# Performance work log

Measured on AMD Instinct MI355X. Metric: run time of the kernel, lower is better.

Reference implementation:

```python
import jax, jax.numpy as jnp
import numpy as np

EPS = 1e-6  # ieps_ln_default
B, S, H, DI, DO = 4, 4096, 8, 128, 128


def _ln(x, g, b, n_axes):
    """LayerNorm over the last n_axes dims (matches nn.LayerNorm(normalized_shape))."""
    axes = tuple(range(x.ndim - n_axes, x.ndim))
    mu = x.mean(axes, keepdims=True)
    var = x.var(axes, keepdims=True)
    return (x - mu) * jax.lax.rsqrt(var + EPS) * g + b


def setup_inputs() -> dict:
    key = jax.random.key(0)
    ks = jax.random.split(key, 12)
    sd = 0.02
    return {
        "heads_input": jax.random.normal(ks[0], (B, S, H, DI), jnp.float32),
        # GroupLinear trans_hid: per-head (2*DI -> 3*DO)
        "W_hid": jax.random.normal(ks[1], (H, 2 * DI, 3 * DO), jnp.float32) * sd,
        "b_hid": jnp.zeros((H, 3 * DO), jnp.float32),
        # normer_csum LN over (H, DI)
        "g_csum": jnp.ones((H, DI), jnp.float32),
        "beta_csum": jnp.zeros((H, DI), jnp.float32),
        # normer_hid LN over (H, 3, DO)
        "g_hid": jnp.ones((H, 3, DO), jnp.float32),
        "beta_hid": jnp.zeros((H, 3, DO), jnp.float32),
        # GroupLinear trans_og: per-head (DI + DO -> DO)
        "W_og": jax.random.normal(ks[2], (H, DI + DO, DO), jnp.float32) * sd,
        "b_og": jnp.zeros((H, DO), jnp.float32),
        # LN inside trans_og over (H, DO)
        "g_og": jnp.ones((H, DO), jnp.float32),
        "beta_og": jnp.zeros((H, DO), jnp.float32),
        "init_cx": jnp.zeros((H, DO), jnp.float32),
    }


def reference(heads_input, W_hid, b_hid, g_csum, beta_csum, g_hid, beta_hid,
              W_og, b_og, g_og, beta_og, init_cx):
    b, s, n, d = heads_input.shape
    # exclusive cumulative sum over seq: cat(zeros, x[:, :-1]).cumsum(1)
    csum = jnp.cumsum(heads_input, axis=1) - heads_input
    csum = _ln(csum, g_csum, beta_csum, 2)
    # grouped (per-head) linear producing igate/fgate/hidden
    x = jnp.concatenate([heads_input, csum], axis=-1)              # [b,s,n,2*d]
    h3 = jnp.einsum('bsni,nio->bsno', x, W_hid) + b_hid            # [b,s,n,3*do]
    do = h3.shape[-1] // 3
    h3 = _ln(h3.reshape(b, s, n, 3, do), g_hid, beta_hid, 3)
    igate, fgate, hidden = h3[..., 0, :], h3[..., 1, :], h3[..., 2, :]
    fg = jax.nn.sigmoid(fgate)
    igh = jax.nn.sigmoid(igate) * jax.nn.relu(hidden)
    # linear recurrence cell_t = fg_t * cell_{t-1} + igh_t  (LGateFunc, dim=1)
    c0 = jnp.broadcast_to(init_cx, (b, n, do))

    def step(c, fi):
        f, i = fi
        c = f * c + i
        return c, c

    _, cell = jax.lax.scan(step, c0, (jnp.swapaxes(fg, 0, 1), jnp.swapaxes(igh, 0, 1)))
    cell = jnp.swapaxes(cell, 0, 1)                                # [b,s,n,do]
    # output gate: GroupLinear + LN, then sigmoid * cell
    og_in = jnp.concatenate([heads_input, cell], axis=-1)
    og = jnp.einsum('bsni,nio->bsno', og_in, W_og) + b_og
    og = _ln(og, g_og, beta_og, 2)
    return jax.nn.sigmoid(og) * cell
```

## Files before the change

### kernel.cpp

```cpp
#include <hip/hip_runtime.h>
#include <math.h>

#define BB 4
#define SS 4096
#define HH 8
#define DI 128
#define DOo 128
#define HD 1024
#define NTOK (BB*SS)
#define LNEPS 1e-6f

#define CS1 32
#define NC1 128
#define CS2 128
#define NC2 32

typedef unsigned short ubf;
typedef __attribute__((ext_vector_type(8))) short    bf16x8;
typedef __attribute__((ext_vector_type(8))) unsigned short u16x8;
typedef __attribute__((ext_vector_type(4))) unsigned short u16x4;
typedef __attribute__((ext_vector_type(4))) float    f32x4;

__device__ __forceinline__ float bf2f(ubf x) {
    union { unsigned int u; float f; } v; v.u = ((unsigned int)x) << 16; return v.f;
}
__device__ __forceinline__ ubf f2bf(float f) {
    union { float f; unsigned int u; } v; v.f = f;
    unsigned int r = v.u + 0x7FFFu + ((v.u >> 16) & 1u);
    return (ubf)(r >> 16);
}
__device__ __forceinline__ float fast_sigmoid(float x) {
    return __builtin_amdgcn_rcpf(1.f + __expf(-x));
}
__device__ __forceinline__ void gload16(const ubf* g, ubf* l) {
    __builtin_amdgcn_global_load_lds(
        (const __attribute__((address_space(1))) void*)g,
        (__attribute__((address_space(3))) void*)l, 16, 0, 0);
}

__global__ void kwt_pack(const float* __restrict__ W, ubf* __restrict__ Wtp, int NB) {
    int bid = blockIdx.x;
    int ks = bid & 7;
    int ns = (bid >> 3) % (NB >> 6);
    int h  = bid / (8 * (NB >> 6));
    int t = threadIdx.x;
    int j = t >> 6, lane = t & 63;
    int n  = ns * 64 + j * 16 + (lane & 15);
    int k0 = ks * 32 + (lane >> 4) * 8;
    u16x8 o;
    #pragma unroll
    for (int e = 0; e < 8; ++e)
        o[e] = f2bf(W[((size_t)h * 256 + k0 + e) * NB + n]);
    *(u16x8*)(Wtp + ((((size_t)(h * (NB >> 6) + ns) * 8 + ks) * 4 + j) * 64 + lane) * 8) = o;
}

__global__ void k1_chunksum(const float* __restrict__ in, float* __restrict__ chunk,
                            ubf* __restrict__ in_bf) {
    int bid = blockIdx.x;
    int c = bid % NC1;
    int h = (bid / NC1) % HH;
    int b = bid / (NC1 * HH);
    int d = threadIdx.x;
    size_t base = (size_t)(b * SS + c * CS1) * HD + h * DI + d;
    float s = 0.f;
    for (int i = 0; i < CS1; ++i) {
        float v = in[base + (size_t)i * HD];
        in_bf[base + (size_t)i * HD] = f2bf(v);
        s += v;
    }
    chunk[((b * NC1 + c) * HH + h) * DI + d] = s;
}

__global__ void k2_chunkscan(float* __restrict__ chunk) {
    int bid = blockIdx.x;
    int h = bid % HH;
    int b = bid / HH;
    int d = threadIdx.x;
    float run = 0.f;
    for (int c0 = 0; c0 < NC1; c0 += 16) {
        float v[16];
        #pragma unroll
        for (int k = 0; k < 16; ++k)
            v[k] = chunk[((b * NC1 + c0 + k) * HH + h) * DI + d];
        #pragma unroll
        for (int k = 0; k < 16; ++k) {
            int idx = ((b * NC1 + c0 + k) * HH + h) * DI + d;
            chunk[idx] = run;
            run += v[k];
        }
    }
}

__global__ void __launch_bounds__(256) k3_csum_ln(
        const float* __restrict__ in, const float* __restrict__ chunkpre,
        const float* __restrict__ g, const float* __restrict__ beta,
        ubf* __restrict__ out) {
    __shared__ float2 scr[2][4];
    int c = blockIdx.x % NC1;
    int b = blockIdx.x / NC1;
    int t = threadIdx.x;
    int lane = t & 63, w = t >> 6;
    int d0 = t * 4;
    f32x4 run = *(const f32x4*)(chunkpre + (size_t)(b * NC1 + c) * HD + d0);
    f32x4 gg  = *(const f32x4*)(g + d0);
    f32x4 bb  = *(const f32x4*)(beta + d0);
    const float* pin = in + (size_t)(b * SS + c * CS1) * HD + d0;
    ubf* pout = out + (size_t)(b * SS + c * CS1) * HD + d0;

    f32x4 v = *(const f32x4*)(pin);
    for (int i = 0; i < CS1; ++i) {
        f32x4 cs = run;
        run += v;
        float s = cs[0] + cs[1] + cs[2] + cs[3];
        float q = cs[0]*cs[0] + cs[1]*cs[1] + cs[2]*cs[2] + cs[3]*cs[3];
        #pragma unroll
        for (int off = 32; off >= 1; off >>= 1) {
            s += __shfl_xor(s, off);
            q += __shfl_xor(q, off);
        }
        if (lane == 0) scr[i & 1][w] = make_float2(s, q);
        if (i + 1 < CS1) v = *(const f32x4*)(pin + (size_t)(i + 1) * HD);
        __syncthreads();
        float2 p0 = scr[i & 1][0], p1 = scr[i & 1][1];
        float2 p2 = scr[i & 1][2], p3 = scr[i & 1][3];
        float S = p0.x + p1.x + p2.x + p3.x;
        float Q = p0.y + p1.y + p2.y + p3.y;
        float mu = S * (1.f / 1024.f);
        float r = rsqrtf(Q * (1.f / 1024.f) - mu * mu + LNEPS);
        u16x4 o;
        #pragma unroll
        for (int e = 0; e < 4; ++e) o[e] = f2bf((cs[e] - mu) * r * gg[e] + bb[e]);
        *(u16x4*)(pout + (size_t)i * HD) = o;
    }
}

template <int NB>
__global__ void __launch_bounds__(256, 2) gemm_h(
        const ubf* __restrict__ Ab0, const ubf* __restrict__ Ab1,
        const ubf* __restrict__ Wtp, const float* __restrict__ bias,
        ubf* __restrict__ C) {
    __shared__ __align__(16) ubf As[64 * 512];
    constexpr int ntiles = NB >> 7;
    int t = threadIdx.x;
    int lane = t & 63, w = t >> 6;
    int h = blockIdx.x & 7;
    int tok0 = (blockIdx.x >> 3) * 128;
    int crs = NB * HH;
    int rl = lane & 15, kq = lane >> 4;

    {
        int rowi = lane >> 4;
        #pragma unroll
        for (int q = 0; q < 16; ++q) {
            int bi = w * 16 + q;
            int rowgrp = bi >> 1, half = bi & 1;
            int row = rowgrp * 4 + rowi;
            int cg = (lane & 15) ^ rowi ^ ((rowgrp & 3) << 2);
            const ubf* src = (half ? Ab1 : Ab0)
                             + (size_t)(tok0 + row) * HD + h * DI + cg * 8;
            gload16(src, As + bi * 512);
        }
    }
    __syncthreads();

    const ubf* pWb = Wtp + ((size_t)h * (NB >> 6)) * 16384 + (size_t)lane * 8;

    #pragma unroll
    for (int nt = 0; nt < ntiles; ++nt) {
        int ns = nt * 2 + (w >> 1);
        bf16x8 bfr[8][4];
        #pragma unroll
        for (int ks = 0; ks < 8; ++ks)
            #pragma unroll
            for (int j = 0; j < 4; ++j)
                bfr[ks][j] = *(const bf16x8*)(pWb + (size_t)((ns * 8 + ks) * 4 + j) * 512);

        f32x4 acc[4][4];
        #pragma unroll
        for (int i = 0; i < 4; ++i)
            #pragma unroll
            for (int j = 0; j < 4; ++j) acc[i][j] = (f32x4){0.f, 0.f, 0.f, 0.f};

        #pragma unroll
        for (int ks = 0; ks < 8; ++ks) {
            int c = ks * 4 + kq;
            int chi = (c >> 4) * 512;
            int clo = (((c & 15) ^ (rl & 3)) ^ (((rl >> 2) & 3) << 2)) * 8;
            bf16x8 af[4];
            #pragma unroll
            for (int i = 0; i < 4; ++i) {
                int r = (w & 1) * 64 + i * 16 + rl;
                af[i] = *(const bf16x8*)(As + ((r >> 2) * 2) * 512 + chi
                                            + (r & 3) * 128 + clo);
            }
            #pragma unroll
            for (int i = 0; i < 4; ++i)
                #pragma unroll
                for (int j = 0; j < 4; ++j)
                    acc[i][j] = __builtin_amdgcn_mfma_f32_16x16x32_bf16(bfr[ks][j], af[i], acc[i][j], 0, 0, 0);
        }

        int nq0 = nt * 128 + (w >> 1) * 64 + kq * 4;
        #pragma unroll
        for (int j = 0; j < 4; ++j) {
            int n = nq0 + j * 16;
            f32x4 bv = *(const f32x4*)(bias + h * NB + n);
            int col = (n >> 7) * 1024 + h * 128 + (n & 127);
            #pragma unroll
            for (int i = 0; i < 4; ++i) {
                u16x4 o;
                o[0] = f2bf(acc[i][j][0] + bv[0]);
                o[1] = f2bf(acc[i][j][1] + bv[1]);
                o[2] = f2bf(acc[i][j][2] + bv[2]);
                o[3] = f2bf(acc[i][j][3] + bv[3]);
                *(u16x4*)(C + (size_t)(tok0 + (w & 1) * 64 + i * 16 + rl) * crs + col) = o;
            }
        }
    }
}

__global__ void __launch_bounds__(256, 4) k4b_ln_gates(
        const ubf* __restrict__ h3, const float* __restrict__ g,
        const float* __restrict__ beta, ubf* __restrict__ fgl, float* __restrict__ igh) {
    int lane = threadIdx.x & 63;
    int tok  = blockIdx.x * 4 + (threadIdx.x >> 6);
    int c0 = 8 * lane;
    const ubf* p = h3 + (size_t)tok * 3072;

    u16x8 raw[6];
    #pragma unroll
    for (int pp = 0; pp < 3; ++pp) {
        raw[pp * 2 + 0] = *(const u16x8*)(p + pp * 1024 + c0);
        raw[pp * 2 + 1] = *(const u16x8*)(p + pp * 1024 + 512 + c0);
    }
    float sum = 0.f, sq = 0.f;
    #pragma unroll
    for (int s = 0; s < 6; ++s) {
        #pragma unroll
        for (int j = 0; j < 8; ++j) {
            float a = bf2f((ubf)raw[s][j]);
            sum += a; sq = fmaf(a, a, sq);
        }
    }
    #pragma unroll
    for (int m = 32; m >= 1; m >>= 1) {
        sum += __shfl_xor(sum, m);
        sq  += __shfl_xor(sq, m);
    }
    float mu = sum * (1.f / 3072.f);
    float r  = rsqrtf(sq * (1.f / 3072.f) - mu * mu + LNEPS);

    int dd = c0 & 127;
    size_t ob = (size_t)tok * HD + c0;
    #pragma unroll
    for (int q = 0; q < 2; ++q) {
        int hq = (c0 + q * 512) >> 7;
        int gb = hq * 384 + dd;
        f32x4 gv[3][2], bv[3][2];
        #pragma unroll
        for (int pp = 0; pp < 3; ++pp) {
            gv[pp][0] = *(const f32x4*)(g + gb + pp * 128);
            gv[pp][1] = *(const f32x4*)(g + gb + pp * 128 + 4);
            bv[pp][0] = *(const f32x4*)(beta + gb + pp * 128);
            bv[pp][1] = *(const f32x4*)(beta + gb + pp * 128 + 4);
        }
        u16x8 fo;
        f32x4 io0, io1;
        #pragma unroll
        for (int j = 0; j < 8; ++j) {
            float ai = bf2f((ubf)raw[0 + q][j]);
            float af = bf2f((ubf)raw[2 + q][j]);
            float ah = bf2f((ubf)raw[4 + q][j]);
            float li = (ai - mu) * r * gv[0][j >> 2][j & 3] + bv[0][j >> 2][j & 3];
            float lf = (af - mu) * r * gv[1][j >> 2][j & 3] + bv[1][j >> 2][j & 3];
            float lh = (ah - mu) * r * gv[2][j >> 2][j & 3] + bv[2][j >> 2][j & 3];
            fo[j] = f2bf(lf);
            float v = fast_sigmoid(li) * fmaxf(lh, 0.f);
            if (j < 4) io0[j & 3] = v; else io1[j & 3] = v;
        }
        *(u16x8*)(fgl + ob + q * 512) = fo;
        *(f32x4*)(igh + ob + q * 512) = io0;
        *(f32x4*)(igh + ob + q * 512 + 4) = io1;
    }
}

__global__ void k5a_chunkrec(const ubf* __restrict__ fgl, const float* __restrict__ igh,
                             float* __restrict__ Pb, float* __restrict__ Lb) {
    int bid = blockIdx.x;
    int h = bid % HH;
    int c = (bid / HH) % NC2;
    int b = bid / (HH * NC2);
    int d = threadIdx.x;
    size_t base = (size_t)(b * SS + c * CS2) * HD + h * DOo + d;
    float P = 1.f, L = 0.f;
    for (int s = 0; s < CS2; ++s) {
        float f = 1.f / (1.f + expf(-bf2f(fgl[base + (size_t)s * HD])));
        float i = igh[base + (size_t)s * HD];
        L = f * L + i;
        P *= f;
    }
    int o = ((b * NC2 + c) * HH + h) * DOo + d;
    Pb[o] = P;
    Lb[o] = L;
}

__global__ void k5b_carry(const float* __restrict__ Pb, const float* __restrict__ Lb,
                          const float* __restrict__ init_cx, float* __restrict__ cIn) {
    int bid = blockIdx.x;
    int h = bid % HH;
    int b = bid / HH;
    int d = threadIdx.x;
    float c = init_cx[h * DOo + d];
    for (int c0 = 0; c0 < NC2; c0 += 8) {
        float pv[8], lv[8];
        #pragma unroll
        for (int k = 0; k < 8; ++k) {
            int o = ((b * NC2 + c0 + k) * HH + h) * DOo + d;
            pv[k] = Pb[o];
            lv[k] = Lb[o];
        }
        #pragma unroll
        for (int k = 0; k < 8; ++k) {
            int o = ((b * NC2 + c0 + k) * HH + h) * DOo + d;
            cIn[o] = c;
            c = pv[k] * c + lv[k];
        }
    }
}

__global__ void k5c_cell(const ubf* __restrict__ fgl, float* __restrict__ igh_cell,
                         const float* __restrict__ cIn, ubf* __restrict__ cell_bf) {
    int bid = blockIdx.x;
    int h = bid % HH;
    int c = (bid / HH) % NC2;
    int b = bid / (HH * NC2);
    int d = threadIdx.x;
    size_t base = (size_t)(b * SS + c * CS2) * HD + h * DOo + d;
    int o = ((b * NC2 + c) * HH + h) * DOo + d;
    float cv = cIn[o];
    for (int s = 0; s < CS2; ++s) {
        float f = 1.f / (1.f + expf(-bf2f(fgl[base + (size_t)s * HD])));
        float i = igh_cell[base + (size_t)s * HD];
        cv = f * cv + i;
        igh_cell[base + (size_t)s * HD] = cv;
        cell_bf[base + (size_t)s * HD] = f2bf(cv);
    }
}

__global__ void __launch_bounds__(256, 4) k6b_ln_out(
        const ubf* __restrict__ ogr, float* __restrict__ out ,
        const float* __restrict__ g, const float* __restrict__ beta) {
    int lane = threadIdx.x & 63;
    int tok  = blockIdx.x * 4 + (threadIdx.x >> 6);
    int c0 = 8 * lane;
    size_t base = (size_t)tok * HD + c0;

    u16x8 og0 = *(const u16x8*)(ogr + base);
    u16x8 og1 = *(const u16x8*)(ogr + base + 512);
    f32x4 cl[2][2];
    cl[0][0] = *(const f32x4*)(out + base);
    cl[0][1] = *(const f32x4*)(out + base + 4);
    cl[1][0] = *(const f32x4*)(out + base + 512);
    cl[1][1] = *(const f32x4*)(out + base + 512 + 4);

    float sum = 0.f, sq = 0.f;
    #pragma unroll
    for (int j = 0; j < 8; ++j) {
        float a0 = bf2f((ubf)og0[j]);
        float a1 = bf2f((ubf)og1[j]);
        sum += a0 + a1;
        sq = fmaf(a0, a0, sq);
        sq = fmaf(a1, a1, sq);
    }
    #pragma unroll
    for (int m = 32; m >= 1; m >>= 1) {
        sum += __shfl_xor(sum, m);
        sq  += __shfl_xor(sq, m);
    }
    float mu = sum * (1.f / 1024.f);
    float r  = rsqrtf(sq * (1.f / 1024.f) - mu * mu + LNEPS);

    #pragma unroll
    for (int q = 0; q < 2; ++q) {
        f32x4 gv0 = *(const f32x4*)(g + q * 512 + c0);
        f32x4 gv1 = *(const f32x4*)(g + q * 512 + c0 + 4);
        f32x4 bv0 = *(const f32x4*)(beta + q * 512 + c0);
        f32x4 bv1 = *(const f32x4*)(beta + q * 512 + c0 + 4);
        f32x4 o0, o1;
        #pragma unroll
        for (int j = 0; j < 8; ++j) {
            float a = bf2f((ubf)(q ? og1[j] : og0[j]));
            float gg = (j < 4) ? gv0[j & 3] : gv1[j & 3];
            float bb = (j < 4) ? bv0[j & 3] : bv1[j & 3];
            float lo = (a - mu) * r * gg + bb;
            float v = fast_sigmoid(lo) * cl[q][j >> 2][j & 3];
            if (j < 4) o0[j & 3] = v; else o1[j & 3] = v;
        }
        *(f32x4*)(out + base + q * 512) = o0;
        *(f32x4*)(out + base + q * 512 + 4) = o1;
    }
}

extern "C" void kernel_launch(void* const* d_in, const int* in_sizes, int n_in,
                              void* d_out, int out_size, void* d_ws, size_t ws_size,
                              hipStream_t stream) {
    const float* heads_input = (const float*)d_in[0];
    const float* W_hid   = (const float*)d_in[1];
    const float* b_hid   = (const float*)d_in[2];
    const float* g_csum  = (const float*)d_in[3];
    const float* beta_csum = (const float*)d_in[4];
    const float* g_hid   = (const float*)d_in[5];
    const float* beta_hid = (const float*)d_in[6];
    const float* W_og    = (const float*)d_in[7];
    const float* b_og    = (const float*)d_in[8];
    const float* g_og    = (const float*)d_in[9];
    const float* beta_og = (const float*)d_in[10];
    const float* init_cx = (const float*)d_in[11];
    float* out = (float*)d_out;

    char* ws = (char*)d_ws;
    ubf* in_bf   = (ubf*)ws;
    ubf* csln_bf = (ubf*)(ws + (size_t)33554432);
    ubf* big     = (ubf*)(ws + (size_t)67108864);
    float* chunk = (float*)big;
    ubf* h3      = big;
    ubf* cell_bf = big;
    ubf* og_bf   = big + (size_t)NTOK * HD;
    char* tail   = ws + (size_t)167772160;
    float* Pb    = (float*)tail;
    float* Lb    = Pb + (size_t)BB * NC2 * HD;
    float* cIn   = Lb + (size_t)BB * NC2 * HD;
    ubf* Wt_hid  = (ubf*)(cIn + (size_t)BB * NC2 * HD);
    ubf* Wt_og   = Wt_hid + (size_t)HH * 384 * 256;
    ubf* fgl     = csln_bf;

    kwt_pack<<<HH * (384 >> 6) * 8, 256, 0, stream>>>(W_hid, Wt_hid, 384);
    kwt_pack<<<HH * (128 >> 6) * 8, 256, 0, stream>>>(W_og, Wt_og, 128);
    k1_chunksum<<<BB * HH * NC1, 128, 0, stream>>>(heads_input, chunk, in_bf);
    k2_chunkscan<<<BB * HH, 128, 0, stream>>>(chunk);
    k3_csum_ln<<<BB * NC1, 256, 0, stream>>>(heads_input, chunk, g_csum, beta_csum, csln_bf);
    gemm_h<384><<<(NTOK / 128) * HH, 256, 0, stream>>>(in_bf, csln_bf, Wt_hid, b_hid, h3);
    k4b_ln_gates<<<NTOK / 4, 256, 0, stream>>>(h3, g_hid, beta_hid, fgl, out);
    k5a_chunkrec<<<BB * NC2 * HH, 128, 0, stream>>>(fgl, out, Pb, Lb);
    k5b_carry<<<BB * HH, 128, 0, stream>>>(Pb, Lb, init_cx, cIn);
    k5c_cell<<<BB * NC2 * HH, 128, 0, stream>>>(fgl, out, cIn, cell_bf);
    gemm_h<128><<<(NTOK / 128) * HH, 256, 0, stream>>>(in_bf, cell_bf, Wt_og, b_og, og_bf);
    k6b_ln_out<<<NTOK / 4, 256, 0, stream>>>(og_bf, out, g_og, beta_og);
}
```

Before: 407.6 us.

## Shrink GEMM token tile, double-buffer weight fragments, reuse bf16 cell in output

```diff
diff --git a/kernel.cpp b/kernel.cpp
--- a/kernel.cpp
+++ b/kernel.cpp
@@ -135,24 +135,25 @@
 }
 
 template <int NB>
-__global__ void __launch_bounds__(256, 2) gemm_h(
+__global__ void __launch_bounds__(256, 4) gemm_h(
         const ubf* __restrict__ Ab0, const ubf* __restrict__ Ab1,
         const ubf* __restrict__ Wtp, const float* __restrict__ bias,
         ubf* __restrict__ C) {
-    __shared__ __align__(16) ubf As[64 * 512];
+    __shared__ __align__(16) ubf As[32 * 512];
     constexpr int ntiles = NB >> 7;
     int t = threadIdx.x;
     int lane = t & 63, w = t >> 6;
     int h = blockIdx.x & 7;
-    int tok0 = (blockIdx.x >> 3) * 128;
+    int tok0 = (blockIdx.x >> 3) * 64;
     int crs = NB * HH;
     int rl = lane & 15, kq = lane >> 4;
+    int wm = w & 1, wn = w >> 1;
 
     {
         int rowi = lane >> 4;
         #pragma unroll
-        for (int q = 0; q < 16; ++q) {
-            int bi = w * 16 + q;
+        for (int q = 0; q < 8; ++q) {
+            int bi = w * 8 + q;
             int rowgrp = bi >> 1, half = bi & 1;
             int row = rowgrp * 4 + rowi;
             int cg = (lane & 15) ^ rowi ^ ((rowgrp & 3) << 2);
@@ -167,53 +168,83 @@
 
     #pragma unroll
     for (int nt = 0; nt < ntiles; ++nt) {
-        int ns = nt * 2 + (w >> 1);
-        bf16x8 bfr[8][4];
-        #pragma unroll
-        for (int ks = 0; ks < 8; ++ks)
-            #pragma unroll
-            for (int j = 0; j < 4; ++j)
-                bfr[ks][j] = *(const bf16x8*)(pWb + (size_t)((ns * 8 + ks) * 4 + j) * 512);
-
-        f32x4 acc[4][4];
-        #pragma unroll
-        for (int i = 0; i < 4; ++i)
+        int ns = nt * 2 + wn;
+        f32x4 acc[2][4];
+        #pragma unroll
+        for (int i = 0; i < 2; ++i)
             #pragma unroll
             for (int j = 0; j < 4; ++j) acc[i][j] = (f32x4){0.f, 0.f, 0.f, 0.f};
 
-        #pragma unroll
-        for (int ks = 0; ks < 8; ++ks) {
-            int c = ks * 4 + kq;
-            int chi = (c >> 4) * 512;
-            int clo = (((c & 15) ^ (rl & 3)) ^ (((rl >> 2) & 3) << 2)) * 8;
-            bf16x8 af[4];
-            #pragma unroll
-            for (int i = 0; i < 4; ++i) {
-                int r = (w & 1) * 64 + i * 16 + rl;
-                af[i] = *(const bf16x8*)(As + ((r >> 2) * 2) * 512 + chi
-                                            + (r & 3) * 128 + clo);
+        bf16x8 b0[4], b1[4];
+        #pragma unroll
+        for (int j = 0; j < 4; ++j)
+            b0[j] = *(const bf16x8*)(pWb + (size_t)((ns * 8 + 0) * 4 + j) * 512);
+        #pragma unroll
+        for (int j = 0; j < 4; ++j)
+            b1[j] = *(const bf16x8*)(pWb + (size_t)((ns * 8 + 1) * 4 + j) * 512);
+
+        #pragma unroll
+        for (int ks = 0; ks < 8; ks += 2) {
+            {
+                int c = ks * 4 + kq;
+                int chi = (c >> 4) * 512;
+                int clo = ((c & 15) ^ (rl & 3) ^ ((rl >> 2) << 2)) * 8;
+                bf16x8 af[2];
+                #pragma unroll
+                for (int i = 0; i < 2; ++i) {
+                    int r = wm * 32 + i * 16 + rl;
+                    af[i] = *(const bf16x8*)(As + ((r >> 2) * 2) * 512 + chi
+                                                + (r & 3) * 128 + clo);
+                }
+                #pragma unroll
+                for (int i = 0; i < 2; ++i)
+                    #pragma unroll
+                    for (int j = 0; j < 4; ++j)
+                        acc[i][j] = __builtin_amdgcn_mfma_f32_16x16x32_bf16(b0[j], af[i], acc[i][j], 0, 0, 0);
             }
-            #pragma unroll
-            for (int i = 0; i < 4; ++i)
+            if (ks + 2 < 8) {
                 #pragma unroll
                 for (int j = 0; j < 4; ++j)
-                    acc[i][j] = __builtin_amdgcn_mfma_f32_16x16x32_bf16(bfr[ks][j], af[i], acc[i][j], 0, 0, 0);
-        }
-
-        int nq0 = nt * 128 + (w >> 1) * 64 + kq * 4;
+                    b0[j] = *(const bf16x8*)(pWb + (size_t)((ns * 8 + ks + 2) * 4 + j) * 512);
+            }
+            {
+                int c = (ks + 1) * 4 + kq;
+                int chi = (c >> 4) * 512;
+                int clo = ((c & 15) ^ (rl & 3) ^ ((rl >> 2) << 2)) * 8;
+                bf16x8 af[2];
+                #pragma unroll
+                for (int i = 0; i < 2; ++i) {
+                    int r = wm * 32 + i * 16 + rl;
+                    af[i] = *(const bf16x8*)(As + ((r >> 2) * 2) * 512 + chi
+                                                + (r & 3) * 128 + clo);
+                }
+                #pragma unroll
+                for (int i = 0; i < 2; ++i)
+                    #pragma unroll
+                    for (int j = 0; j < 4; ++j)
+                        acc[i][j] = __builtin_amdgcn_mfma_f32_16x16x32_bf16(b1[j], af[i], acc[i][j], 0, 0, 0);
+            }
+            if (ks + 3 < 8) {
+                #pragma unroll
+                for (int j = 0; j < 4; ++j)
+                    b1[j] = *(const bf16x8*)(pWb + (size_t)((ns * 8 + ks + 3) * 4 + j) * 512);
+            }
+        }
+
+        int nq0 = nt * 128 + wn * 64 + kq * 4;
         #pragma unroll
         for (int j = 0; j < 4; ++j) {
             int n = nq0 + j * 16;
             f32x4 bv = *(const f32x4*)(bias + h * NB + n);
             int col = (n >> 7) * 1024 + h * 128 + (n & 127);
             #pragma unroll
-            for (int i = 0; i < 4; ++i) {
+            for (int i = 0; i < 2; ++i) {
                 u16x4 o;
                 o[0] = f2bf(acc[i][j][0] + bv[0]);
                 o[1] = f2bf(acc[i][j][1] + bv[1]);
                 o[2] = f2bf(acc[i][j][2] + bv[2]);
                 o[3] = f2bf(acc[i][j][3] + bv[3]);
-                *(u16x4*)(C + (size_t)(tok0 + (w & 1) * 64 + i * 16 + rl) * crs + col) = o;
+                *(u16x4*)(C + (size_t)(tok0 + wm * 32 + i * 16 + rl) * crs + col) = o;
             }
         }
     }
@@ -328,7 +359,7 @@
     }
 }
 
-__global__ void k5c_cell(const ubf* __restrict__ fgl, float* __restrict__ igh_cell,
+__global__ void k5c_cell(const ubf* __restrict__ fgl, const float* __restrict__ igh,
                          const float* __restrict__ cIn, ubf* __restrict__ cell_bf) {
     int bid = blockIdx.x;
     int h = bid % HH;
@@ -340,16 +371,15 @@
     float cv = cIn[o];
     for (int s = 0; s < CS2; ++s) {
         float f = 1.f / (1.f + expf(-bf2f(fgl[base + (size_t)s * HD])));
-        float i = igh_cell[base + (size_t)s * HD];
+        float i = igh[base + (size_t)s * HD];
         cv = f * cv + i;
-        igh_cell[base + (size_t)s * HD] = cv;
         cell_bf[base + (size_t)s * HD] = f2bf(cv);
     }
 }
 
 __global__ void __launch_bounds__(256, 4) k6b_ln_out(
-        const ubf* __restrict__ ogr, float* __restrict__ out ,
-        const float* __restrict__ g, const float* __restrict__ beta) {
+        const ubf* __restrict__ ogr, const ubf* __restrict__ cell_bf,
+        float* __restrict__ out, const float* __restrict__ g, const float* __restrict__ beta) {
     int lane = threadIdx.x & 63;
     int tok  = blockIdx.x * 4 + (threadIdx.x >> 6);
     int c0 = 8 * lane;
@@ -357,11 +387,8 @@
 
     u16x8 og0 = *(const u16x8*)(ogr + base);
     u16x8 og1 = *(const u16x8*)(ogr + base + 512);
-    f32x4 cl[2][2];
-    cl[0][0] = *(const f32x4*)(out + base);
-    cl[0][1] = *(const f32x4*)(out + base + 4);
-    cl[1][0] = *(const f32x4*)(out + base + 512);
-    cl[1][1] = *(const f32x4*)(out + base + 512 + 4);
+    u16x8 cb0 = *(const u16x8*)(cell_bf + base);
+    u16x8 cb1 = *(const u16x8*)(cell_bf + base + 512);
 
     float sum = 0.f, sq = 0.f;
     #pragma unroll
@@ -390,10 +417,11 @@
         #pragma unroll
         for (int j = 0; j < 8; ++j) {
             float a = bf2f((ubf)(q ? og1[j] : og0[j]));
+            float cl = bf2f((ubf)(q ? cb1[j] : cb0[j]));
             float gg = (j < 4) ? gv0[j & 3] : gv1[j & 3];
             float bb = (j < 4) ? bv0[j & 3] : bv1[j & 3];
             float lo = (a - mu) * r * gg + bb;
-            float v = fast_sigmoid(lo) * cl[q][j >> 2][j & 3];
+            float v = fast_sigmoid(lo) * cl;
             if (j < 4) o0[j & 3] = v; else o1[j & 3] = v;
         }
         *(f32x4*)(out + base + q * 512) = o0;
@@ -439,11 +467,11 @@
     k1_chunksum<<<BB * HH * NC1, 128, 0, stream>>>(heads_input, chunk, in_bf);
     k2_chunkscan<<<BB * HH, 128, 0, stream>>>(chunk);
     k3_csum_ln<<<BB * NC1, 256, 0, stream>>>(heads_input, chunk, g_csum, beta_csum, csln_bf);
-    gemm_h<384><<<(NTOK / 128) * HH, 256, 0, stream>>>(in_bf, csln_bf, Wt_hid, b_hid, h3);
+    gemm_h<384><<<(NTOK / 64) * HH, 256, 0, stream>>>(in_bf, csln_bf, Wt_hid, b_hid, h3);
     k4b_ln_gates<<<NTOK / 4, 256, 0, stream>>>(h3, g_hid, beta_hid, fgl, out);
     k5a_chunkrec<<<BB * NC2 * HH, 128, 0, stream>>>(fgl, out, Pb, Lb);
     k5b_carry<<<BB * HH, 128, 0, stream>>>(Pb, Lb, init_cx, cIn);
     k5c_cell<<<BB * NC2 * HH, 128, 0, stream>>>(fgl, out, cIn, cell_bf);
-    gemm_h<128><<<(NTOK / 128) * HH, 256, 0, stream>>>(in_bf, cell_bf, Wt_og, b_og, og_bf);
-    k6b_ln_out<<<NTOK / 4, 256, 0, stream>>>(og_bf, out, g_og, beta_og);
-}
+    gemm_h<128><<<(NTOK / 64) * HH, 256, 0, stream>>>(in_bf, cell_bf, Wt_og, b_og, og_bf);
+    k6b_ln_out<<<NTOK / 4, 256, 0, stream>>>(og_bf, cell_bf, out, g_og, beta_og);
+}
```

Result: faster. 391.2 us (-4.0%).

## Store igh as bf16, drop fp32 cell writeback, halve scan chunk size

Applied to the files above, without the earlier changes.

```diff
diff --git a/kernel.cpp b/kernel.cpp
--- a/kernel.cpp
+++ b/kernel.cpp
@@ -12,8 +12,8 @@
 
 #define CS1 32
 #define NC1 128
-#define CS2 128
-#define NC2 32
+#define CS2 64
+#define NC2 64
 
 typedef unsigned short ubf;
 typedef __attribute__((ext_vector_type(8))) short    bf16x8;
@@ -221,7 +221,7 @@
 
 __global__ void __launch_bounds__(256, 4) k4b_ln_gates(
         const ubf* __restrict__ h3, const float* __restrict__ g,
-        const float* __restrict__ beta, ubf* __restrict__ fgl, float* __restrict__ igh) {
+        const float* __restrict__ beta, ubf* __restrict__ fgl, ubf* __restrict__ igh) {
     int lane = threadIdx.x & 63;
     int tok  = blockIdx.x * 4 + (threadIdx.x >> 6);
     int c0 = 8 * lane;
@@ -264,8 +264,7 @@
             bv[pp][0] = *(const f32x4*)(beta + gb + pp * 128);
             bv[pp][1] = *(const f32x4*)(beta + gb + pp * 128 + 4);
         }
-        u16x8 fo;
-        f32x4 io0, io1;
+        u16x8 fo, io;
         #pragma unroll
         for (int j = 0; j < 8; ++j) {
             float ai = bf2f((ubf)raw[0 + q][j]);
@@ -275,16 +274,14 @@
             float lf = (af - mu) * r * gv[1][j >> 2][j & 3] + bv[1][j >> 2][j & 3];
             float lh = (ah - mu) * r * gv[2][j >> 2][j & 3] + bv[2][j >> 2][j & 3];
             fo[j] = f2bf(lf);
-            float v = fast_sigmoid(li) * fmaxf(lh, 0.f);
-            if (j < 4) io0[j & 3] = v; else io1[j & 3] = v;
+            io[j] = f2bf(fast_sigmoid(li) * fmaxf(lh, 0.f));
         }
         *(u16x8*)(fgl + ob + q * 512) = fo;
-        *(f32x4*)(igh + ob + q * 512) = io0;
-        *(f32x4*)(igh + ob + q * 512 + 4) = io1;
-    }
-}
-
-__global__ void k5a_chunkrec(const ubf* __restrict__ fgl, const float* __restrict__ igh,
+        *(u16x8*)(igh + ob + q * 512) = io;
+    }
+}
+
+__global__ void k5a_chunkrec(const ubf* __restrict__ fgl, const ubf* __restrict__ igh,
                              float* __restrict__ Pb, float* __restrict__ Lb) {
     int bid = blockIdx.x;
     int h = bid % HH;
@@ -294,8 +291,8 @@
     size_t base = (size_t)(b * SS + c * CS2) * HD + h * DOo + d;
     float P = 1.f, L = 0.f;
     for (int s = 0; s < CS2; ++s) {
-        float f = 1.f / (1.f + expf(-bf2f(fgl[base + (size_t)s * HD])));
-        float i = igh[base + (size_t)s * HD];
+        float f = fast_sigmoid(bf2f(fgl[base + (size_t)s * HD]));
+        float i = bf2f(igh[base + (size_t)s * HD]);
         L = f * L + i;
         P *= f;
     }
@@ -328,7 +325,7 @@
     }
 }
 
-__global__ void k5c_cell(const ubf* __restrict__ fgl, float* __restrict__ igh_cell,
+__global__ void k5c_cell(const ubf* __restrict__ fgl, const ubf* __restrict__ igh,
                          const float* __restrict__ cIn, ubf* __restrict__ cell_bf) {
     int bid = blockIdx.x;
     int h = bid % HH;
@@ -339,17 +336,16 @@
     int o = ((b * NC2 + c) * HH + h) * DOo + d;
     float cv = cIn[o];
     for (int s = 0; s < CS2; ++s) {
-        float f = 1.f / (1.f + expf(-bf2f(fgl[base + (size_t)s * HD])));
-        float i = igh_cell[base + (size_t)s * HD];
+        float f = fast_sigmoid(bf2f(fgl[base + (size_t)s * HD]));
+        float i = bf2f(igh[base + (size_t)s * HD]);
         cv = f * cv + i;
-        igh_cell[base + (size_t)s * HD] = cv;
         cell_bf[base + (size_t)s * HD] = f2bf(cv);
     }
 }
 
 __global__ void __launch_bounds__(256, 4) k6b_ln_out(
-        const ubf* __restrict__ ogr, float* __restrict__ out ,
-        const float* __restrict__ g, const float* __restrict__ beta) {
+        const ubf* __restrict__ ogr, const ubf* __restrict__ cell_bf,
+        float* __restrict__ out, const float* __restrict__ g, const float* __restrict__ beta) {
     int lane = threadIdx.x & 63;
     int tok  = blockIdx.x * 4 + (threadIdx.x >> 6);
     int c0 = 8 * lane;
@@ -357,11 +353,8 @@
 
     u16x8 og0 = *(const u16x8*)(ogr + base);
     u16x8 og1 = *(const u16x8*)(ogr + base + 512);
-    f32x4 cl[2][2];
-    cl[0][0] = *(const f32x4*)(out + base);
-    cl[0][1] = *(const f32x4*)(out + base + 4);
-    cl[1][0] = *(const f32x4*)(out + base + 512);
-    cl[1][1] = *(const f32x4*)(out + base + 512 + 4);
+    u16x8 cb0 = *(const u16x8*)(cell_bf + base);
+    u16x8 cb1 = *(const u16x8*)(cell_bf + base + 512);
 
     float sum = 0.f, sq = 0.f;
     #pragma unroll
@@ -390,10 +383,11 @@
         #pragma unroll
         for (int j = 0; j < 8; ++j) {
             float a = bf2f((ubf)(q ? og1[j] : og0[j]));
+            float cl = bf2f((ubf)(q ? cb1[j] : cb0[j]));
             float gg = (j < 4) ? gv0[j & 3] : gv1[j & 3];
             float bb = (j < 4) ? bv0[j & 3] : bv1[j & 3];
             float lo = (a - mu) * r * gg + bb;
-            float v = fast_sigmoid(lo) * cl[q][j >> 2][j & 3];
+            float v = fast_sigmoid(lo) * cl;
             if (j < 4) o0[j & 3] = v; else o1[j & 3] = v;
         }
         *(f32x4*)(out + base + q * 512) = o0;
@@ -421,18 +415,20 @@
     char* ws = (char*)d_ws;
     ubf* in_bf   = (ubf*)ws;
     ubf* csln_bf = (ubf*)(ws + (size_t)33554432);
-    ubf* big     = (ubf*)(ws + (size_t)67108864);
-    float* chunk = (float*)big;
+    char* bigc   = ws + (size_t)67108864;
+    ubf* big     = (ubf*)bigc;
+    float* chunk = (float*)bigc;
     ubf* h3      = big;
     ubf* cell_bf = big;
     ubf* og_bf   = big + (size_t)NTOK * HD;
-    char* tail   = ws + (size_t)167772160;
-    float* Pb    = (float*)tail;
+    float* Pb    = (float*)(bigc + (size_t)73400320);
     float* Lb    = Pb + (size_t)BB * NC2 * HD;
     float* cIn   = Lb + (size_t)BB * NC2 * HD;
-    ubf* Wt_hid  = (ubf*)(cIn + (size_t)BB * NC2 * HD);
+    char* tail   = ws + (size_t)167772160;
+    ubf* Wt_hid  = (ubf*)tail;
     ubf* Wt_og   = Wt_hid + (size_t)HH * 384 * 256;
     ubf* fgl     = csln_bf;
+    ubf* igh_bf  = (ubf*)out;
 
     kwt_pack<<<HH * (384 >> 6) * 8, 256, 0, stream>>>(W_hid, Wt_hid, 384);
     kwt_pack<<<HH * (128 >> 6) * 8, 256, 0, stream>>>(W_og, Wt_og, 128);
@@ -440,10 +436,10 @@
     k2_chunkscan<<<BB * HH, 128, 0, stream>>>(chunk);
     k3_csum_ln<<<BB * NC1, 256, 0, stream>>>(heads_input, chunk, g_csum, beta_csum, csln_bf);
     gemm_h<384><<<(NTOK / 128) * HH, 256, 0, stream>>>(in_bf, csln_bf, Wt_hid, b_hid, h3);
-    k4b_ln_gates<<<NTOK / 4, 256, 0, stream>>>(h3, g_hid, beta_hid, fgl, out);
-    k5a_chunkrec<<<BB * NC2 * HH, 128, 0, stream>>>(fgl, out, Pb, Lb);
+    k4b_ln_gates<<<NTOK / 4, 256, 0, stream>>>(h3, g_hid, beta_hid, fgl, igh_bf);
+    k5a_chunkrec<<<BB * NC2 * HH, 128, 0, stream>>>(fgl, igh_bf, Pb, Lb);
     k5b_carry<<<BB * HH, 128, 0, stream>>>(Pb, Lb, init_cx, cIn);
-    k5c_cell<<<BB * NC2 * HH, 128, 0, stream>>>(fgl, out, cIn, cell_bf);
+    k5c_cell<<<BB * NC2 * HH, 128, 0, stream>>>(fgl, igh_bf, cIn, cell_bf);
     gemm_h<128><<<(NTOK / 128) * HH, 256, 0, stream>>>(in_bf, cell_bf, Wt_og, b_og, og_bf);
-    k6b_ln_out<<<NTOK / 4, 256, 0, stream>>>(og_bf, out, g_og, beta_og);
-}
+    k6b_ln_out<<<NTOK / 4, 256, 0, stream>>>(og_bf, cell_bf, out, g_og, beta_og);
+}
```

Result: faster. 341.3 us (-16.3%).
